# Kernel tuning notes

Measured on AMD Instinct MI355X. Metric: run time of the kernel, lower is better.

## Reference

```python
import jax, jax.numpy as jnp
import numpy as np

B, T, D_IN = 128, 1024, 13
H = 256                      # total CfC units (hidden_units)
N_INTER, N_CMD, N_MOTOR = 77, 51, 128   # AutoNCP(256, 128) layer partition
SIZES = (N_INTER, N_CMD, N_MOTOR)
INS = (D_IN, N_INTER, N_CMD)


def setup_inputs() -> dict:
    key = jax.random.key(0)
    ks = iter(jax.random.split(key, 64))

    def w(shape):
        scale = 1.0 / np.sqrt(shape[-1])
        return jax.random.uniform(next(ks), shape, jnp.float32, -scale, scale)

    inp = {}
    inp["x"] = jax.random.normal(next(ks), (B, T, D_IN), dtype=jnp.float32)
    inp["lstm_Wih"] = w((4 * H, D_IN))
    inp["lstm_Whh"] = w((4 * H, H))
    inp["lstm_bih"] = w((4 * H,))
    inp["lstm_bhh"] = w((4 * H,))
    for l, (nin, nh) in enumerate(zip(INS, SIZES)):
        for nm in ("ff1", "ff2", "ta", "tb"):
            inp[f"l{l}_W{nm}"] = w((nh, nin + nh))
            inp[f"l{l}_b{nm}"] = w((nh,))
        # NCP input sparsity (~0.5 density) + all-ones recurrent block, as WiredCfCCell
        m_in = (jax.random.uniform(next(ks), (nh, nin)) < 0.5).astype(jnp.float32)
        inp[f"l{l}_mask"] = jnp.concatenate([m_in, jnp.ones((nh, nh), jnp.float32)], axis=1)
    inp["gyro_W"] = w((3, N_MOTOR)); inp["gyro_b"] = w((3,))
    inp["acc_W"] = w((3, N_MOTOR)); inp["acc_b"] = w((3,))
    inp["unc_W"] = w((6, N_MOTOR)); inp["unc_b"] = w((6,))
    return inp


def _cfc_cell(z, W1, b1, W2, b2, Wa, ba, Wb, bb, mask):
    # CfC cell, "default" mode, no backbone, ts = 1.0 (CfC called without timespans)
    ff1 = jnp.tanh(z @ (W1 * mask).T + b1)
    ff2 = jnp.tanh(z @ (W2 * mask).T + b2)
    t_interp = jax.nn.sigmoid(z @ Wa.T + ba + z @ Wb.T + bb)  # sigmoid(t_a*1 + t_b)
    return ff1 * (1.0 - t_interp) + t_interp * ff2


def _forward(x, lstm_Wih, lstm_Whh, lstm_bih, lstm_bhh, layer_params, masks,
             gyro_W, gyro_b, acc_W, acc_b, unc_W, unc_b):
    bsz = x.shape[0]
    h0 = jnp.zeros((bsz, H), x.dtype)
    c0 = jnp.zeros((bsz, H), x.dtype)
    b_lstm = lstm_bih + lstm_bhh

    def step(carry, x_t):
        h, c = carry
        # mixed-memory LSTM cell on the full state
        gates = x_t @ lstm_Wih.T + h @ lstm_Whh.T + b_lstm
        i, f, g, o = jnp.split(gates, 4, axis=-1)
        c = jax.nn.sigmoid(f) * c + jax.nn.sigmoid(i) * jnp.tanh(g)
        h = jax.nn.sigmoid(o) * jnp.tanh(c)
        # WiredCfCCell: sequential NCP layers (inter -> command -> motor)
        hs = (h[:, :N_INTER], h[:, N_INTER:N_INTER + N_CMD], h[:, N_INTER + N_CMD:])
        inp = x_t
        new_hs = []
        for l in range(3):
            inp = _cfc_cell(jnp.concatenate([inp, hs[l]], axis=-1), *layer_params[l], masks[l])
            new_hs.append(inp)
        h = jnp.concatenate(new_hs, axis=-1)
        return (h, c), new_hs[-1]

    _, motor = jax.lax.scan(step, (h0, c0), jnp.swapaxes(x, 0, 1))
    motor = jnp.swapaxes(motor, 0, 1)  # (B, T, N_MOTOR)
    pred = jnp.concatenate([motor @ gyro_W.T + gyro_b, motor @ acc_W.T + acc_b], axis=-1)
    uncertainty = jax.nn.softplus(motor @ unc_W.T + unc_b)
    return pred, uncertainty


def reference(x, lstm_Wih, lstm_Whh, lstm_bih, lstm_bhh,
              l0_Wff1, l0_bff1, l0_Wff2, l0_bff2, l0_Wta, l0_bta, l0_Wtb, l0_btb, l0_mask,
              l1_Wff1, l1_bff1, l1_Wff2, l1_bff2, l1_Wta, l1_bta, l1_Wtb, l1_btb, l1_mask,
              l2_Wff1, l2_bff1, l2_Wff2, l2_bff2, l2_Wta, l2_bta, l2_Wtb, l2_btb, l2_mask,
              gyro_W, gyro_b, acc_W, acc_b, unc_W, unc_b):
    layer_params = (
        (l0_Wff1, l0_bff1, l0_Wff2, l0_bff2, l0_Wta, l0_bta, l0_Wtb, l0_btb),
        (l1_Wff1, l1_bff1, l1_Wff2, l1_bff2, l1_Wta, l1_bta, l1_Wtb, l1_btb),
        (l2_Wff1, l2_bff1, l2_Wff2, l2_bff2, l2_Wta, l2_bta, l2_Wtb, l2_btb),
    )
    masks = (l0_mask, l1_mask, l2_mask)
    return _forward(x, lstm_Wih, lstm_Whh, lstm_bih, lstm_bhh, layer_params, masks,
                    gyro_W, gyro_b, acc_W, acc_b, unc_W, unc_b)
```

## Files before the change

### kernel.cpp

```cpp
#include <hip/hip_runtime.h>
#include <cstdint>

#define B_  128
#define T_  1024
#define DIN 13
#define HS  256
#define N0  77
#define N1  51
#define N2  128

#define QG   34
#define NRG  1024
#define Q0   12
#define NR0  308
#define Q1   16
#define NR1  204
#define Q2   23
#define NR2  512
#define Q2LDS 18

#define EXSTRIDE 320
#define X1O   0
#define X2O   128
#define F1O   256
#define F2O   272

typedef _Float16 h2_t __attribute__((ext_vector_type(2)));

static __device__ __forceinline__ uint32_t pk2(float a, float b) {
  h2_t v; v.x = (_Float16)a; v.y = (_Float16)b;
  return __builtin_bit_cast(uint32_t, v);
}
static __device__ __forceinline__ unsigned short f16b(float v) {
  return __builtin_bit_cast(unsigned short, (_Float16)v);
}
static __device__ __forceinline__ void st16(void* base, int idx, unsigned short v) {
  ((unsigned short*)base)[idx] = v;
}
static __device__ __forceinline__ float dot2f(uint32_t w, uint32_t z, float acc) {
#if __has_builtin(__builtin_amdgcn_fdot2)
  return __builtin_amdgcn_fdot2(__builtin_bit_cast(h2_t, w), __builtin_bit_cast(h2_t, z), acc, false);
#else
  h2_t a = __builtin_bit_cast(h2_t, w), b = __builtin_bit_cast(h2_t, z);
  return acc + (float)a.x * (float)b.x + (float)a.y * (float)b.y;
#endif
}
static __device__ __forceinline__ float dot8f(uint4 w, uint4 z, float acc) {
  acc = dot2f(w.x, z.x, acc);
  acc = dot2f(w.y, z.y, acc);
  acc = dot2f(w.z, z.z, acc);
  acc = dot2f(w.w, z.w, acc);
  return acc;
}
static __device__ __forceinline__ float sigf(float x) { return 1.f / (1.f + expf(-x)); }

static __device__ __forceinline__ void axstore(int* p, float v) {
  __hip_atomic_store(p, __builtin_bit_cast(int, v), __ATOMIC_RELAXED, __HIP_MEMORY_SCOPE_AGENT);
}
static __device__ __forceinline__ void axstorei(int* p, int v) {
  __hip_atomic_store(p, v, __ATOMIC_RELAXED, __HIP_MEMORY_SCOPE_AGENT);
}
static __device__ __forceinline__ float axload(const int* p) {
  return __builtin_bit_cast(float, __hip_atomic_load((int*)p, __ATOMIC_RELAXED, __HIP_MEMORY_SCOPE_AGENT));
}
static __device__ __forceinline__ void vmw() {
  asm volatile("s_waitcnt vmcnt(0)" ::: "memory");
}
static __device__ __forceinline__ void flag_wait(const int* p, int v) {
  while (__hip_atomic_load((int*)p, __ATOMIC_RELAXED, __HIP_MEMORY_SCOPE_AGENT) < v)
    __builtin_amdgcn_s_sleep(1);
}


__global__ void prep_gates3(const float* __restrict__ Wih, const float* __restrict__ Whh,
                            uint32_t* __restrict__ out) {
  int id = blockIdx.x * blockDim.x + threadIdx.x;
  if (id >= 136 * NRG) return;
  int k2 = id >> 10, row = id & (NRG - 1);
  float v[2];
#pragma unroll
  for (int j = 0; j < 2; ++j) {
    int e = 2 * k2 + j;
    float val = 0.f;
    if (e < 13) val = Wih[row * DIN + e];
    else if (e >= 16 && e < 144) val = Whh[row * HS + 128 + (e - 16)];
    else if (e >= 144 && e < 195) val = Whh[row * HS + 77 + (e - 144)];
    else if (e >= 195 && e < 272) val = Whh[row * HS + (e - 195)];
    v[j] = val;
  }
  out[((k2 >> 2) * NRG + row) * 4 + (k2 & 3)] = pk2(v[0], v[1]);
}

__global__ void prep_cfc2(const float* __restrict__ Wf1, const float* __restrict__ Wf2,
                          const float* __restrict__ Wta, const float* __restrict__ Wtb,
                          const float* __restrict__ mask,
                          int nh, int K, int NR, int K2,
                          int p0n, int p0c, int p1s, int p1n, int p1c,
                          uint32_t* __restrict__ out) {
  int id = blockIdx.x * blockDim.x + threadIdx.x;
  if (id >= NR * K2) return;
  int k2 = id / NR, r = id % NR;
  int mat = r / nh, o = r % nh;
  const float* W = (mat == 0) ? Wf1 : (mat == 1) ? Wf2 : (mat == 2) ? Wta : Wtb;
  float v[2];
#pragma unroll
  for (int j = 0; j < 2; ++j) {
    int e = 2 * k2 + j;
    int col = -1;
    if (e < p0n) col = p0c + e;
    else if (e >= p1s && e < p1s + p1n) col = p1c + (e - p1s);
    float val = 0.f;
    if (col >= 0) {
      val = W[o * K + col];
      if (mat < 2) val *= mask[o * K + col];
    }
    v[j] = val;
  }
  out[((k2 >> 2) * NR + r) * 4 + (k2 & 3)] = pk2(v[0], v[1]);
}


struct SMA {
  uint4 l0w[Q0 * NR0];
  uint4 l1w[Q1 * NR1];
  uint4 zb[2][QG];
  uint4 z0[Q0];
  uint4 z1[Q1];
  float garr[512];
  float ffb[NR0];
  float cb0[NR0];
  float cb1[NR1];
};
struct SMB {
  uint4 l2w[Q2LDS * NR2];
  uint4 zb[2][QG];
  uint4 z2[Q2];
  float garr[512];
  float ffb[NR2];
  float cb2[NR2];
  uint4 hwq[12][16];
  float hb[12];
};
static_assert(sizeof(SMA) <= 163840, "SMA too big");
static_assert(sizeof(SMB) <= 163840, "SMB too big");

struct PArgs {
  const float* x;
  const float* bih; const float* bhh;
  const float* b0[4]; const float* b1[4]; const float* b2[4];
  const float* gW; const float* gb; const float* aW; const float* ab;
  const float* uW; const float* ub;
  const uint4* wsG; const uint4* wsL0; const uint4* wsL1; const uint4* wsL2;
  int* ex;
  float* out;
};

__global__ __launch_bounds__(512, 2) void rnn_coop2(PArgs P) {
  extern __shared__ char smraw[];
  const int tid = threadIdx.x;
  const bool isA = (blockIdx.x < B_);
  const int b = blockIdx.x & (B_ - 1);
  int* EX = P.ex + b * EXSTRIDE;
  int* F1 = EX + F1O;
  int* F2 = EX + F2O;
  const float* xb = P.x + (size_t)b * T_ * DIN;
  const size_t UNC_OFF = (size_t)B_ * T_ * 6;

  if (isA) {
    SMA& sm = *(SMA*)smraw;
    for (int i = tid; i < Q0 * NR0; i += 512) sm.l0w[i] = P.wsL0[i];
    for (int i = tid; i < Q1 * NR1; i += 512) sm.l1w[i] = P.wsL1[i];
    for (int i = tid; i < NR0; i += 512) sm.cb0[i] = P.b0[i / N0][i % N0];
    for (int i = tid; i < NR1; i += 512) sm.cb1[i] = P.b1[i / N1][i % N1];
    {
      uint32_t* zz = (uint32_t*)sm.zb;
      for (int i = tid; i < (2 * QG + Q0 + Q1) * 4; i += 512) zz[i] = 0u;
    }
    const int grow = ((tid >> 7) << 8) | (tid & 127);
    const float bg = P.bih[grow] + P.bhh[grow];
    float c_r = 0.f;
    __syncthreads();
    if (tid < 13) {
      unsigned short v = f16b(xb[tid]);
      st16(sm.zb[0], tid, v);
      st16(sm.z0, tid, v);
    }
    __syncthreads();
    float acc = bg;
    acc = dot8f(P.wsG[0 * NRG + grow], sm.zb[0][0], acc);
    acc = dot8f(P.wsG[1 * NRG + grow], sm.zb[0][1], acc);
    uint4* zbc = sm.zb[0];
    uint4* zbn = sm.zb[1];

    for (int t = 0; t < T_; ++t) {
#pragma unroll 8
      for (int q = 2; q < 18; ++q)
        acc = dot8f(P.wsG[q * NRG + grow], zbc[q], acc);
      sm.garr[tid] = acc;
      __syncthreads();
      if (tid < 128) {
        float gi = sm.garr[tid], gf = sm.garr[128 + tid];
        float gg = sm.garr[256 + tid], go = sm.garr[384 + tid];
        float cn = sigf(gf) * c_r + sigf(gi) * tanhf(gg);
        c_r = cn;
        float h = sigf(go) * tanhf(cn);
        if (tid < N0) st16(sm.z0, 13 + tid, f16b(h));
        else          st16(sm.z1, tid - N0, f16b(h));
      } else if (tid >= 320 && tid < 336) {
        int i = tid - 320;
        if (i < 13) {
          float xv = (t + 1 < T_) ? xb[(size_t)(t + 1) * DIN + i] : 0.f;
          st16(zbn, i, f16b(xv));
        }
      } else if (tid >= 336 && tid < 352) {
        int i = tid - 336;
        if (i < 13) st16(sm.z0, i, ((unsigned short*)zbc)[i]);
      }
      __syncthreads();
      if (tid < NR0) {
        float a = sm.cb0[tid];
#pragma unroll
        for (int q = 0; q < Q0; ++q) a = dot8f(sm.l0w[q * NR0 + tid], sm.z0[q], a);
        sm.ffb[tid] = (tid < 2 * N0) ? tanhf(a) : a;
      }
      __syncthreads();
      if (tid < N0) {
        float ti = sigf(sm.ffb[2 * N0 + tid] + sm.ffb[3 * N0 + tid]);
        float v = sm.ffb[tid] * (1.f - ti) + ti * sm.ffb[N0 + tid];
        unsigned short v16 = f16b(v);
        st16(sm.z1, 51 + tid, v16);
        st16(zbn, 195 + tid, v16);
        axstore(EX + X1O + tid, v);
      }
      __syncthreads();
      if (tid < NR1) {
        float a = sm.cb1[tid];
#pragma unroll
        for (int q = 0; q < Q1; ++q) a = dot8f(sm.l1w[q * NR1 + tid], sm.z1[q], a);
        sm.ffb[tid] = (tid < 2 * N1) ? tanhf(a) : a;
      }
      __syncthreads();
      if (tid < N1) {
        float ti = sigf(sm.ffb[2 * N1 + tid] + sm.ffb[3 * N1 + tid]);
        float v = sm.ffb[tid] * (1.f - ti) + ti * sm.ffb[N1 + tid];
        st16(zbn, 144 + tid, f16b(v));
        axstore(EX + X1O + N0 + tid, v);
      }
      vmw();
      __syncthreads();
      if (tid == 0) axstorei(F1, t + 1);
      acc = bg;
      acc = dot8f(P.wsG[0 * NRG + grow], zbn[0], acc);
      acc = dot8f(P.wsG[1 * NRG + grow], zbn[1], acc);
#pragma unroll 8
      for (int q = 18; q < 34; ++q)
        acc = dot8f(P.wsG[q * NRG + grow], zbn[q], acc);
      flag_wait(F2, t + 1);
      if (tid < 128) st16(zbn, 16 + tid, f16b(axload(EX + X2O + tid)));
      __syncthreads();
      uint4* tmp = zbc; zbc = zbn; zbn = tmp;
    }
  } else {
    SMB& sm = *(SMB*)smraw;
    for (int i = tid; i < Q2LDS * NR2; i += 512) sm.l2w[i] = P.wsL2[i];
    for (int i = tid; i < NR2; i += 512) sm.cb2[i] = P.b2[i >> 7][i & 127];
    for (int i = tid; i < 768; i += 512) {
      int r = i >> 6, w = i & 63;
      const float* W = (r < 3) ? P.gW + r * 128 : (r < 6) ? P.aW + (r - 3) * 128 : P.uW + (r - 6) * 128;
      ((uint32_t*)sm.hwq)[i] = pk2(W[2 * w], W[2 * w + 1]);
    }
    if (tid < 12) sm.hb[tid] = (tid < 3) ? P.gb[tid] : (tid < 6) ? P.ab[tid - 3] : P.ub[tid - 6];
    {
      uint32_t* zz = (uint32_t*)sm.zb;
      for (int i = tid; i < (2 * QG + Q2) * 4; i += 512) zz[i] = 0u;
    }
    const int grow = ((tid >> 7) << 8) | 128 | (tid & 127);
    const float bg = P.bih[grow] + P.bhh[grow];
    float c_r = 0.f;
    __syncthreads();
    if (tid < 13) st16(sm.zb[0], tid, f16b(xb[tid]));
    __syncthreads();
    uint4* zbc = sm.zb[0];
    uint4* zbn = sm.zb[1];

    for (int t = 0; t < T_; ++t) {
      float acc = bg;
      if (tid < 12 && t > 0) {
        int r = tid;
        float a = sm.hb[r];
#pragma unroll
        for (int q = 0; q < 16; ++q) a = dot8f(sm.hwq[r][q], zbc[2 + q], a);
        size_t base = ((size_t)b * T_ + (t - 1)) * 6;
        if (r < 6) P.out[base + r] = a;
        else {
          float sp = (a > 0.f) ? (a + log1pf(expf(-a))) : log1pf(expf(a));
          P.out[UNC_OFF + base + (r - 6)] = sp;
        }
      }
#pragma unroll 8
      for (int q = 0; q < QG; ++q)
        acc = dot8f(P.wsG[q * NRG + grow], zbc[q], acc);
      sm.garr[tid] = acc;
      __syncthreads();
      if (tid < 128) {
        float gi = sm.garr[tid], gf = sm.garr[128 + tid];
        float gg = sm.garr[256 + tid], go = sm.garr[384 + tid];
        float cn = sigf(gf) * c_r + sigf(gi) * tanhf(gg);
        c_r = cn;
        float h = sigf(go) * tanhf(cn);
        st16(sm.z2, 56 + tid, f16b(h));
      } else if (tid >= 192 && tid < 208) {
        int i = tid - 192;
        if (i < 13) {
          float xv = (t + 1 < T_) ? xb[(size_t)(t + 1) * DIN + i] : 0.f;
          st16(zbn, i, f16b(xv));
        }
      }
      __syncthreads();
      float a2 = sm.cb2[tid];
#pragma unroll
      for (int q = 7; q < Q2LDS; ++q) a2 = dot8f(sm.l2w[q * NR2 + tid], sm.z2[q], a2);
#pragma unroll
      for (int q = Q2LDS; q < Q2; ++q) a2 = dot8f(P.wsL2[q * NR2 + tid], sm.z2[q], a2);
      flag_wait(F1, t + 1);
      if (tid < N0) {
        st16(zbn, 195 + tid, f16b(axload(EX + X1O + tid)));
      } else if (tid < 128) {
        int j = tid - N0;
        float v = axload(EX + X1O + N0 + j);
        unsigned short v16 = f16b(v);
        st16(sm.z2, j, v16);
        st16(zbn, 144 + j, v16);
      }
      __syncthreads();
#pragma unroll
      for (int q = 0; q < 7; ++q) a2 = dot8f(sm.l2w[q * NR2 + tid], sm.z2[q], a2);
      sm.ffb[tid] = (tid < 2 * N2) ? tanhf(a2) : a2;
      __syncthreads();
      if (tid < N2) {
        float ti = sigf(sm.ffb[2 * N2 + tid] + sm.ffb[3 * N2 + tid]);
        float v = sm.ffb[tid] * (1.f - ti) + ti * sm.ffb[N2 + tid];
        st16(zbn, 16 + tid, f16b(v));
        axstore(EX + X2O + tid, v);
      }
      vmw();
      __syncthreads();
      if (tid == 0) axstorei(F2, t + 1);
      uint4* tmp = zbc; zbc = zbn; zbn = tmp;
    }
    if (tid < 12) {
      int r = tid;
      float a = sm.hb[r];
#pragma unroll
      for (int q = 0; q < 16; ++q) a = dot8f(sm.hwq[r][q], zbc[2 + q], a);
      size_t base = ((size_t)b * T_ + (T_ - 1)) * 6;
      if (r < 6) P.out[base + r] = a;
      else {
        float sp = (a > 0.f) ? (a + log1pf(expf(-a))) : log1pf(expf(a));
        P.out[UNC_OFF + base + (r - 6)] = sp;
      }
    }
  }
}


struct Args {
  const float* x;
  const float* Wih; const float* Whh; const float* bih; const float* bhh;
  const float* W0[4]; const float* b0[4]; const float* m0;
  const float* W1[4]; const float* b1[4]; const float* m1;
  const float* W2[4]; const float* b2[4]; const float* m2;
  const float* gW; const float* gb; const float* aW; const float* ab;
  const float* uW; const float* ub;
  float* out;
};

struct SMF {
  float xt[16];
  float lstm_h[HS];
  float hprev[HS];
  float garr[4 * HS];
  float ffb[4][128];
  float cb0[NR0];
  float cb1[NR1];
  float cb2[NR2];
  float hw[12][132];
  float hb[12];
};

__global__ __launch_bounds__(512, 2) void rnn_fallback(Args A) {
  extern __shared__ char smraw[];
  SMF& sm = *(SMF*)smraw;
  const int tid = threadIdx.x;
  const int b = blockIdx.x;

  for (int i = tid; i < NR0; i += 512) sm.cb0[i] = A.b0[i / N0][i % N0];
  for (int i = tid; i < NR1; i += 512) sm.cb1[i] = A.b1[i / N1][i % N1];
  for (int i = tid; i < NR2; i += 512) sm.cb2[i] = A.b2[i / N2][i % N2];
  for (int i = tid; i < 12 * 128; i += 512) {
    int r = i >> 7, k = i & 127;
    sm.hw[r][k] = (r < 3) ? A.gW[r * 128 + k]
                : (r < 6) ? A.aW[(r - 3) * 128 + k]
                          : A.uW[(r - 6) * 128 + k];
  }
  if (tid < 12) sm.hb[tid] = (tid < 3) ? A.gb[tid] : (tid < 6) ? A.ab[tid - 3] : A.ub[tid - 6];
  for (int i = tid; i < HS; i += 512) sm.hprev[i] = 0.f;
  float bga = A.bih[tid] + A.bhh[tid];
  float bgb = A.bih[tid + 512] + A.bhh[tid + 512];
  float c_r = 0.f;
  __syncthreads();

  const float* xb = A.x + (size_t)b * T_ * DIN;
  const size_t UNC_OFF = (size_t)B_ * T_ * 6;

  for (int t = 0; t < T_; ++t) {
    const float* xp = xb + (size_t)t * DIN;
    if (tid < DIN) sm.xt[tid] = xp[tid];
    __syncthreads();

    float aa = bga, ab = bgb;
    for (int k = 0; k < DIN; ++k) {
      float xv = sm.xt[k];
      aa += A.Wih[tid * DIN + k] * xv;
      ab += A.Wih[(tid + 512) * DIN + k] * xv;
    }
    for (int k = 0; k < HS; ++k) {
      float hv = sm.hprev[k];
      aa += A.Whh[tid * HS + k] * hv;
      ab += A.Whh[(tid + 512) * HS + k] * hv;
    }
    sm.garr[tid] = aa;
    sm.garr[tid + 512] = ab;
    __syncthreads();

    if (tid < HS) {
      float gi = sm.garr[tid], gf = sm.garr[HS + tid];
      float gg = sm.garr[2 * HS + tid], go = sm.garr[3 * HS + tid];
      float cn = sigf(gf) * c_r + sigf(gi) * tanhf(gg);
      c_r = cn;
      sm.lstm_h[tid] = sigf(go) * tanhf(cn);
    }
    __syncthreads();

    if (tid < NR0) {
      int mat = tid / N0, o = tid % N0;
      const float* W = A.W0[mat];
      const float* m = A.m0;
      const int Kl = DIN + N0;
      float acc = sm.cb0[tid];
      for (int k = 0; k < DIN; ++k) {
        float w = W[o * Kl + k];
        if (mat < 2) w *= m[o * Kl + k];
        acc += w * sm.xt[k];
      }
      for (int k = DIN; k < Kl; ++k) acc += W[o * Kl + k] * sm.lstm_h[k - DIN];
      sm.ffb[mat][o] = (mat < 2) ? tanhf(acc) : acc;
    }
    __syncthreads();
    if (tid < N0) {
      float ti = sigf(sm.ffb[2][tid] + sm.ffb[3][tid]);
      sm.hprev[tid] = sm.ffb[0][tid] * (1.f - ti) + ti * sm.ffb[1][tid];
    }
    __syncthreads();

    if (tid < NR1) {
      int mat = tid / N1, o = tid % N1;
      const float* W = A.W1[mat];
      const float* m = A.m1;
      const int Kl = N0 + N1;
      float acc = sm.cb1[tid];
      for (int k = 0; k < N0; ++k) {
        float w = W[o * Kl + k];
        if (mat < 2) w *= m[o * Kl + k];
        acc += w * sm.hprev[k];
      }
      for (int k = N0; k < Kl; ++k) acc += W[o * Kl + k] * sm.lstm_h[k];
      sm.ffb[mat][o] = (mat < 2) ? tanhf(acc) : acc;
    }
    __syncthreads();
    if (tid < N1) {
      float ti = sigf(sm.ffb[2][tid] + sm.ffb[3][tid]);
      sm.hprev[N0 + tid] = sm.ffb[0][tid] * (1.f - ti) + ti * sm.ffb[1][tid];
    }
    __syncthreads();

    {
      int mat = tid >> 7, o = tid & 127;
      const float* W = A.W2[mat];
      const float* m = A.m2;
      const int Kl = N1 + N2;
      float acc = sm.cb2[tid];
      for (int k = 0; k < N1; ++k) {
        float w = W[o * Kl + k];
        if (mat < 2) w *= m[o * Kl + k];
        acc += w * sm.hprev[N0 + k];
      }
      for (int k = N1; k < Kl; ++k) acc += W[o * Kl + k] * sm.lstm_h[N0 + k];
      sm.ffb[mat][o] = (mat < 2) ? tanhf(acc) : acc;
    }
    __syncthreads();
    if (tid < N2) {
      float ti = sigf(sm.ffb[2][tid] + sm.ffb[3][tid]);
      sm.hprev[N0 + N1 + tid] = sm.ffb[0][tid] * (1.f - ti) + ti * sm.ffb[1][tid];
    }
    __syncthreads();

    if (tid >= 256 && tid < 268) {
      int r = tid - 256;
      const float* mo = &sm.hprev[N0 + N1];
      float acc = sm.hb[r];
      for (int k = 0; k < 128; ++k) acc += sm.hw[r][k] * mo[k];
      size_t base = ((size_t)b * T_ + t) * 6;
      if (r < 6) A.out[base + r] = acc;
      else {
        float sp = (acc > 0.f) ? (acc + log1pf(expf(-acc))) : log1pf(expf(acc));
        A.out[UNC_OFF + base + (r - 6)] = sp;
      }
    }
    __syncthreads();
  }
}


extern "C" void kernel_launch(void* const* d_in, const int* in_sizes, int n_in,
                              void* d_out, int out_size, void* d_ws, size_t ws_size,
                              hipStream_t stream) {
  const float* x   = (const float*)d_in[0];
  const float* Wih = (const float*)d_in[1];
  const float* Whh = (const float*)d_in[2];
  const float* bih = (const float*)d_in[3];
  const float* bhh = (const float*)d_in[4];
  const float *W[3][4], *bb[3][4], *mk[3];
  for (int l = 0; l < 3; ++l) {
    int base = 5 + l * 9;
    for (int nm = 0; nm < 4; ++nm) {
      W[l][nm]  = (const float*)d_in[base + 2 * nm];
      bb[l][nm] = (const float*)d_in[base + 2 * nm + 1];
    }
    mk[l] = (const float*)d_in[base + 8];
  }
  const float* gW = (const float*)d_in[32];
  const float* gb = (const float*)d_in[33];
  const float* aW = (const float*)d_in[34];
  const float* ab = (const float*)d_in[35];
  const float* uW = (const float*)d_in[36];
  const float* ub = (const float*)d_in[37];

  char* ws = (char*)d_ws;
  const size_t szG  = (size_t)QG * NRG * 16;
  const size_t szL0 = (size_t)Q0 * NR0 * 16;
  const size_t szL1 = (size_t)Q1 * NR1 * 16;
  const size_t szL2 = (size_t)Q2 * NR2 * 16;
  const size_t offG = 0, offL0 = szG, offL1 = offL0 + szL0, offL2 = offL1 + szL1;
  const size_t offEx = offL2 + szL2;
  const size_t exBytes = (size_t)B_ * EXSTRIDE * 4;
  const size_t need = offEx + exBytes;

  if (ws_size >= need) {
    PArgs P;
    P.x = x; P.bih = bih; P.bhh = bhh;
    for (int nm = 0; nm < 4; ++nm) { P.b0[nm] = bb[0][nm]; P.b1[nm] = bb[1][nm]; P.b2[nm] = bb[2][nm]; }
    P.gW = gW; P.gb = gb; P.aW = aW; P.ab = ab; P.uW = uW; P.ub = ub;
    P.wsG  = (const uint4*)(ws + offG);
    P.wsL0 = (const uint4*)(ws + offL0);
    P.wsL1 = (const uint4*)(ws + offL1);
    P.wsL2 = (const uint4*)(ws + offL2);
    P.ex   = (int*)(ws + offEx);
    P.out  = (float*)d_out;

    hipMemsetAsync(ws + offEx, 0, exBytes, stream);
    int n;
    n = 136 * NRG;
    prep_gates3<<<(n + 255) / 256, 256, 0, stream>>>(Wih, Whh, (uint32_t*)(ws + offG));
    n = NR0 * 48;
    prep_cfc2<<<(n + 255) / 256, 256, 0, stream>>>(W[0][0], W[0][1], W[0][2], W[0][3], mk[0],
                                                   N0, DIN + N0, NR0, 48,
                                                   90, 0, 96, 0, 0,
                                                   (uint32_t*)(ws + offL0));
    n = NR1 * 64;
    prep_cfc2<<<(n + 255) / 256, 256, 0, stream>>>(W[1][0], W[1][1], W[1][2], W[1][3], mk[1],
                                                   N1, N0 + N1, NR1, 64,
                                                   51, 77, 51, 77, 0,
                                                   (uint32_t*)(ws + offL1));
    n = NR2 * 92;
    prep_cfc2<<<(n + 255) / 256, 256, 0, stream>>>(W[2][0], W[2][1], W[2][2], W[2][3], mk[2],
                                                   N2, N1 + N2, NR2, 92,
                                                   51, 0, 56, 128, 51,
                                                   (uint32_t*)(ws + offL2));
    int lds = (int)((sizeof(SMA) > sizeof(SMB)) ? sizeof(SMA) : sizeof(SMB));
    hipFuncSetAttribute(reinterpret_cast<const void*>(&rnn_coop2),
                        hipFuncAttributeMaxDynamicSharedMemorySize, lds);
    rnn_coop2<<<2 * B_, 512, lds, stream>>>(P);
    return;
  }

  Args A;
  A.x = x; A.Wih = Wih; A.Whh = Whh; A.bih = bih; A.bhh = bhh;
  for (int nm = 0; nm < 4; ++nm) {
    A.W0[nm] = W[0][nm]; A.b0[nm] = bb[0][nm];
    A.W1[nm] = W[1][nm]; A.b1[nm] = bb[1][nm];
    A.W2[nm] = W[2][nm]; A.b2[nm] = bb[2][nm];
  }
  A.m0 = mk[0]; A.m1 = mk[1]; A.m2 = mk[2];
  A.gW = gW; A.gb = gb; A.aW = aW; A.ab = ab; A.uW = uW; A.ub = ub;
  A.out = (float*)d_out;
  hipFuncSetAttribute(reinterpret_cast<const void*>(&rnn_fallback),
                      hipFuncAttributeMaxDynamicSharedMemorySize, (int)sizeof(SMF));
  rnn_fallback<<<B_, 512, sizeof(SMF), stream>>>(A);
}
```

Before: 5.964 ms.

## Replace flag-based inter-block handoff with tagged per-element publish/poll

Inter-block exchange now packs each fp16 value with a step tag in one 32-bit word. Consumers poll each element until its tag matches, which replaces the separate flag word, the vmcnt wait and the extra barrier before raising the flag. Block A also prefetches its gate weights into registers and reorders the gate dot products so only the part that depends on layer 2 waits on the poll. Block B moves its gate matvec ahead of the head output. The cost is more register pressure, busy polling without sleep, and reliance on tags not aliasing, which holds since tags stay below 65536.

```diff
diff --git a/kernel.cpp b/kernel.cpp
--- a/kernel.cpp
+++ b/kernel.cpp
@@ -19,11 +19,9 @@
 #define NR2  512
 #define Q2LDS 18
 
-#define EXSTRIDE 320
+#define EXSTRIDE 256
 #define X1O   0
 #define X2O   128
-#define F1O   256
-#define F2O   272
 
 typedef _Float16 h2_t __attribute__((ext_vector_type(2)));
 
@@ -54,21 +52,15 @@
 }
 static __device__ __forceinline__ float sigf(float x) { return 1.f / (1.f + expf(-x)); }
 
-static __device__ __forceinline__ void axstore(int* p, float v) {
-  __hip_atomic_store(p, __builtin_bit_cast(int, v), __ATOMIC_RELAXED, __HIP_MEMORY_SCOPE_AGENT);
-}
-static __device__ __forceinline__ void axstorei(int* p, int v) {
-  __hip_atomic_store(p, v, __ATOMIC_RELAXED, __HIP_MEMORY_SCOPE_AGENT);
-}
-static __device__ __forceinline__ float axload(const int* p) {
-  return __builtin_bit_cast(float, __hip_atomic_load((int*)p, __ATOMIC_RELAXED, __HIP_MEMORY_SCOPE_AGENT));
-}
-static __device__ __forceinline__ void vmw() {
-  asm volatile("s_waitcnt vmcnt(0)" ::: "memory");
-}
-static __device__ __forceinline__ void flag_wait(const int* p, int v) {
-  while (__hip_atomic_load((int*)p, __ATOMIC_RELAXED, __HIP_MEMORY_SCOPE_AGENT) < v)
-    __builtin_amdgcn_s_sleep(1);
+static __device__ __forceinline__ void axpub(int* p, int tag, unsigned short v16) {
+  __hip_atomic_store(p, (tag << 16) | (int)v16, __ATOMIC_RELAXED, __HIP_MEMORY_SCOPE_AGENT);
+}
+static __device__ __forceinline__ unsigned short axpoll(const int* p, int tag) {
+  int w;
+  do {
+    w = __hip_atomic_load((int*)p, __ATOMIC_RELAXED, __HIP_MEMORY_SCOPE_AGENT);
+  } while (((unsigned)w >> 16) != (unsigned)tag);
+  return (unsigned short)(w & 0xFFFF);
 }
 
 
@@ -155,14 +147,12 @@
   float* out;
 };
 
-__global__ __launch_bounds__(512, 2) void rnn_coop2(PArgs P) {
+__global__ __launch_bounds__(512, 2) void rnn_coop3(PArgs P) {
   extern __shared__ char smraw[];
   const int tid = threadIdx.x;
   const bool isA = (blockIdx.x < B_);
   const int b = blockIdx.x & (B_ - 1);
   int* EX = P.ex + b * EXSTRIDE;
-  int* F1 = EX + F1O;
-  int* F2 = EX + F2O;
   const float* xb = P.x + (size_t)b * T_ * DIN;
   const size_t UNC_OFF = (size_t)B_ * T_ * 6;
 
@@ -180,24 +170,19 @@
     const float bg = P.bih[grow] + P.bhh[grow];
     float c_r = 0.f;
     __syncthreads();
-    if (tid < 13) {
-      unsigned short v = f16b(xb[tid]);
-      st16(sm.zb[0], tid, v);
-      st16(sm.z0, tid, v);
-    }
-    __syncthreads();
-    float acc = bg;
-    acc = dot8f(P.wsG[0 * NRG + grow], sm.zb[0][0], acc);
-    acc = dot8f(P.wsG[1 * NRG + grow], sm.zb[0][1], acc);
+    if (tid < 13) st16(sm.zb[0], tid, f16b(xb[tid]));
+    __syncthreads();
     uint4* zbc = sm.zb[0];
     uint4* zbn = sm.zb[1];
+    {
+      float acc = bg;
+      acc = dot8f(P.wsG[0 * NRG + grow], zbc[0], acc);
+      acc = dot8f(P.wsG[1 * NRG + grow], zbc[1], acc);
+      sm.garr[tid] = acc;
+    }
+    __syncthreads();
 
     for (int t = 0; t < T_; ++t) {
-#pragma unroll 8
-      for (int q = 2; q < 18; ++q)
-        acc = dot8f(P.wsG[q * NRG + grow], zbc[q], acc);
-      sm.garr[tid] = acc;
-      __syncthreads();
       if (tid < 128) {
         float gi = sm.garr[tid], gf = sm.garr[128 + tid];
         float gg = sm.garr[256 + tid], go = sm.garr[384 + tid];
@@ -228,9 +213,9 @@
         float ti = sigf(sm.ffb[2 * N0 + tid] + sm.ffb[3 * N0 + tid]);
         float v = sm.ffb[tid] * (1.f - ti) + ti * sm.ffb[N0 + tid];
         unsigned short v16 = f16b(v);
+        axpub(EX + X1O + tid, t + 1, v16);
         st16(sm.z1, 51 + tid, v16);
         st16(zbn, 195 + tid, v16);
-        axstore(EX + X1O + tid, v);
       }
       __syncthreads();
       if (tid < NR1) {
@@ -243,20 +228,29 @@
       if (tid < N1) {
         float ti = sigf(sm.ffb[2 * N1 + tid] + sm.ffb[3 * N1 + tid]);
         float v = sm.ffb[tid] * (1.f - ti) + ti * sm.ffb[N1 + tid];
-        st16(zbn, 144 + tid, f16b(v));
-        axstore(EX + X1O + N0 + tid, v);
-      }
-      vmw();
-      __syncthreads();
-      if (tid == 0) axstorei(F1, t + 1);
-      acc = bg;
+        unsigned short v16 = f16b(v);
+        axpub(EX + X1O + N0 + tid, t + 1, v16);
+        st16(zbn, 144 + tid, v16);
+      }
+      __syncthreads();
+      uint4 pw[16];
+#pragma unroll
+      for (int q = 0; q < 16; ++q) pw[q] = P.wsG[(2 + q) * NRG + grow];
+      float acc = bg;
       acc = dot8f(P.wsG[0 * NRG + grow], zbn[0], acc);
       acc = dot8f(P.wsG[1 * NRG + grow], zbn[1], acc);
 #pragma unroll 8
       for (int q = 18; q < 34; ++q)
         acc = dot8f(P.wsG[q * NRG + grow], zbn[q], acc);
-      flag_wait(F2, t + 1);
-      if (tid < 128) st16(zbn, 16 + tid, f16b(axload(EX + X2O + tid)));
+      asm volatile("" ::: "memory");
+      if (tid < 128) {
+        unsigned short v16 = axpoll(EX + X2O + tid, t + 1);
+        st16(zbn, 16 + tid, v16);
+      }
+      __syncthreads();
+#pragma unroll
+      for (int q = 0; q < 16; ++q) acc = dot8f(pw[q], zbn[2 + q], acc);
+      sm.garr[tid] = acc;
       __syncthreads();
       uint4* tmp = zbc; zbc = zbn; zbn = tmp;
     }
@@ -285,6 +279,9 @@
 
     for (int t = 0; t < T_; ++t) {
       float acc = bg;
+#pragma unroll 8
+      for (int q = 0; q < QG; ++q)
+        acc = dot8f(P.wsG[q * NRG + grow], zbc[q], acc);
       if (tid < 12 && t > 0) {
         int r = tid;
         float a = sm.hb[r];
@@ -297,9 +294,6 @@
           P.out[UNC_OFF + base + (r - 6)] = sp;
         }
       }
-#pragma unroll 8
-      for (int q = 0; q < QG; ++q)
-        acc = dot8f(P.wsG[q * NRG + grow], zbc[q], acc);
       sm.garr[tid] = acc;
       __syncthreads();
       if (tid < 128) {
@@ -322,15 +316,15 @@
       for (int q = 7; q < Q2LDS; ++q) a2 = dot8f(sm.l2w[q * NR2 + tid], sm.z2[q], a2);
 #pragma unroll
       for (int q = Q2LDS; q < Q2; ++q) a2 = dot8f(P.wsL2[q * NR2 + tid], sm.z2[q], a2);
-      flag_wait(F1, t + 1);
-      if (tid < N0) {
-        st16(zbn, 195 + tid, f16b(axload(EX + X1O + tid)));
-      } else if (tid < 128) {
-        int j = tid - N0;
-        float v = axload(EX + X1O + N0 + j);
-        unsigned short v16 = f16b(v);
-        st16(sm.z2, j, v16);
-        st16(zbn, 144 + j, v16);
+      if (tid < 128) {
+        unsigned short v16 = axpoll(EX + X1O + tid, t + 1);
+        if (tid < N0) {
+          st16(zbn, 195 + tid, v16);
+        } else {
+          int j = tid - N0;
+          st16(sm.z2, j, v16);
+          st16(zbn, 144 + j, v16);
+        }
       }
       __syncthreads();
 #pragma unroll
@@ -340,12 +334,11 @@
       if (tid < N2) {
         float ti = sigf(sm.ffb[2 * N2 + tid] + sm.ffb[3 * N2 + tid]);
         float v = sm.ffb[tid] * (1.f - ti) + ti * sm.ffb[N2 + tid];
-        st16(zbn, 16 + tid, f16b(v));
-        axstore(EX + X2O + tid, v);
-      }
-      vmw();
-      __syncthreads();
-      if (tid == 0) axstorei(F2, t + 1);
+        unsigned short v16 = f16b(v);
+        axpub(EX + X2O + tid, t + 1, v16);
+        st16(zbn, 16 + tid, v16);
+      }
+      __syncthreads();
       uint4* tmp = zbc; zbc = zbn; zbn = tmp;
     }
     if (tid < 12) {
@@ -588,9 +581,9 @@
                                                    51, 0, 56, 128, 51,
                                                    (uint32_t*)(ws + offL2));
     int lds = (int)((sizeof(SMA) > sizeof(SMB)) ? sizeof(SMA) : sizeof(SMB));
-    hipFuncSetAttribute(reinterpret_cast<const void*>(&rnn_coop2),
+    hipFuncSetAttribute(reinterpret_cast<const void*>(&rnn_coop3),
                         hipFuncAttributeMaxDynamicSharedMemorySize, lds);
-    rnn_coop2<<<2 * B_, 512, lds, stream>>>(P);
+    rnn_coop3<<<2 * B_, 512, lds, stream>>>(P);
     return;
   }
 
```

After: 5.430 ms. 9.0% less time.
